# Kernel tuning notes

Hardware: AMD Instinct MI355X
Metric: run time of the kernel (lower is better)

The kernel has to match this reference:

```python
import jax, jax.numpy as jnp
import numpy as np

N, DIM, DK, DV = 8192, 1024, 128, 128


def setup_inputs() -> dict:
    key = jax.random.key(0)
    ks = jax.random.split(key, 5)
    # Match equinox Linear init scale roughly (uniform(-1/sqrt(in), 1/sqrt(in)))
    lim = 1.0 / np.sqrt(DIM)
    return {
        "x": jax.random.normal(ks[0], (N, DIM), dtype=jnp.float32),
        "Wqk": jax.random.uniform(ks[1], (DK, DIM), jnp.float32, -lim, lim),
        "bqk": jax.random.uniform(ks[2], (DK,), jnp.float32, -lim, lim),
        "Wv": jax.random.uniform(ks[3], (DV, DIM), jnp.float32, -lim, lim),
        "bv": jax.random.uniform(ks[4], (DV,), jnp.float32, -lim, lim),
    }


def reference(x, Wqk, bqk, Wv, bv):
    # shared QK projection: q == k == x @ Wqk^T + bqk  -> [n, dk]
    qk = jnp.einsum("nd,kd->nk", x, Wqk) + bqk
    v = jnp.einsum("nd,vd->nv", x, Wv) + bv  # [n, dv]
    # full n x n score matrix (no 1/sqrt(dk) scaling in the original)
    score = jnp.einsum("ik,jk->ij", qk, qk)  # [n, n]
    score = jax.nn.softmax(score, axis=-1)
    return jnp.einsum("ij,jv->iv", score, v)  # [n, dv]
```

## Files before the change

kernel.cpp:

```cpp
#include <hip/hip_runtime.h>
#include <math.h>

#define NROWS 8192
#define DIMX  1024
#define DKV   128
#define KSPLIT 4
#define KEYS_PER_SPLIT (NROWS / KSPLIT)
#define BN 64
#define QK_SCALE 1.2011224087864498f
#define M_FIX 96.0f

typedef __attribute__((ext_vector_type(8))) short bf16x8;
typedef __attribute__((ext_vector_type(4))) short s16x4;
typedef __attribute__((ext_vector_type(4))) float f32x4;

static __device__ __forceinline__ short f2bf(float f) {
    union { float f; unsigned u; } v; v.f = f;
    unsigned r = v.u + 0x7fff + ((v.u >> 16) & 1);
    return (short)(r >> 16);
}

__global__ __launch_bounds__(256) void wcvt_kernel(
    const float* __restrict__ Wqk, const float* __restrict__ bqk,
    const float* __restrict__ Wv,  const float* __restrict__ bv,
    short* __restrict__ wb, float* __restrict__ bb)
{
    const int idx = blockIdx.x * 1024 + threadIdx.x * 4;
    const bool isqk = idx < DKV * DIMX;
    const float* src = isqk ? (Wqk + idx) : (Wv + (idx - DKV * DIMX));
    const float sc = isqk ? QK_SCALE : 1.0f;
    const float4 f = *(const float4*)src;
    s16x4 o;
    o.x = f2bf(f.x * sc); o.y = f2bf(f.y * sc);
    o.z = f2bf(f.z * sc); o.w = f2bf(f.w * sc);
    *(s16x4*)&wb[idx] = o;
    if (blockIdx.x == 0) {
        const int t = threadIdx.x;
        bb[t] = (t < DKV) ? bqk[t] * QK_SCALE : bv[t - DKV];
    }
}

__global__ __launch_bounds__(256) void proj_kernel(
    const float* __restrict__ x, const short* __restrict__ wb,
    const float* __restrict__ bb, short* __restrict__ qkb, short* __restrict__ vtb)
{
    __shared__ __align__(16) short xb[32 * 1024];

    const int tid  = threadIdx.x;
    const int lane = tid & 63;
    const int wave = tid >> 6;
    const int l15  = lane & 15;
    const int quad = lane >> 4;
    const int mat  = blockIdx.y;
    const int rbase = blockIdx.x * 32;
    const int wr = wave >> 1, wc = wave & 1;
    const short* wsrc = wb + (size_t)mat * DKV * DIMX;

    #pragma unroll 8
    for (int i = 0; i < 32; ++i) {
        const float4 f = *(const float4*)(x + (size_t)(rbase + i) * DIMX + tid * 4);
        s16x4 o;
        o.x = f2bf(f.x); o.y = f2bf(f.y); o.z = f2bf(f.z); o.w = f2bf(f.w);
        *(s16x4*)&xb[i * 1024 + ((tid * 4) ^ ((i & 7) << 3))] = o;
    }
    __syncthreads();

    f32x4 acc[4];
    for (int i = 0; i < 4; ++i) acc[i] = (f32x4)0.0f;

    const int arow = wr * 16 + l15;
    const int aswz = (arow & 7) << 3;
    const short* arowp = &xb[arow * 1024];

    #pragma unroll 2
    for (int kk = 0; kk < 32; ++kk) {
        const bf16x8 a = *(const bf16x8*)&arowp[(kk * 32 + quad * 8) ^ aswz];
        for (int nt = 0; nt < 4; ++nt) {
            const int col = wc * 64 + nt * 16 + l15;
            const bf16x8 b = *(const bf16x8*)(wsrc + (size_t)col * DIMX + kk * 32 + quad * 8);
            acc[nt] = __builtin_amdgcn_mfma_f32_16x16x32_bf16(a, b, acc[nt], 0, 0, 0);
        }
    }

    const int rw = rbase + wr * 16 + quad * 4;
    for (int nt = 0; nt < 4; ++nt) {
        const int col = wc * 64 + nt * 16 + l15;
        const float bias = bb[mat * DKV + col];
        if (mat == 0) {
            for (int r = 0; r < 4; ++r)
                qkb[(size_t)(rw + r) * DKV + col] = f2bf(acc[nt][r] + bias);
        } else {
            s16x4 o;
            o.x = f2bf(acc[nt][0] + bias); o.y = f2bf(acc[nt][1] + bias);
            o.z = f2bf(acc[nt][2] + bias); o.w = f2bf(acc[nt][3] + bias);
            *(s16x4*)&vtb[(size_t)col * NROWS + rw] = o;
        }
    }
}

__global__ __launch_bounds__(256, 2) void flash_kernel(
    const short* __restrict__ qkb, const short* __restrict__ vtb,
    float* __restrict__ opart, float* __restrict__ lpart)
{
    __shared__ __align__(16) short kt[2][64 * 128];
    __shared__ __align__(16) short vt[2][128 * 64];
    __shared__ __align__(16) short pb[4][32 * 64];

    const int tid  = threadIdx.x;
    const int lane = tid & 63;
    const int wave = tid >> 6;
    const int l15  = lane & 15;
    const int quad = lane >> 4;
    const int rg   = wave >> 1;
    const int kh   = wave & 1;
    const int rbase = blockIdx.x * 64 + rg * 32;
    const int ks = blockIdx.y;
    const int swzr = (l15 & 7) << 3;

    unsigned koff[4], voff[4];
    for (int i = 0; i < 4; ++i) {
        const int krow = wave * 16 + i * 4 + quad;
        koff[i] = (unsigned)krow * 256u
                + (((unsigned)l15 * 16u) ^ (((unsigned)krow & 7u) << 4));
        const int vrow = wave * 32 + i * 8 + (lane >> 3);
        voff[i] = (unsigned)vrow * (unsigned)(NROWS * 2)
                + ((((unsigned)lane & 7u) * 16u) ^ (((unsigned)vrow & 7u) << 4));
    }

#define FL_ISSUE(buf, j0) do { \
        const char* kb_ = (const char*)qkb + (size_t)(j0) * (DKV * 2); \
        const char* vb_ = (const char*)vtb + (size_t)(j0) * 2; \
        for (int i = 0; i < 4; ++i) \
            __builtin_amdgcn_global_load_lds( \
                (const __attribute__((address_space(1))) void*)(kb_ + koff[i]), \
                (__attribute__((address_space(3))) void*)((char*)&kt[buf][0] + (wave * 4 + i) * 1024), \
                16, 0, 0); \
        for (int i = 0; i < 4; ++i) \
            __builtin_amdgcn_global_load_lds( \
                (const __attribute__((address_space(1))) void*)(vb_ + voff[i]), \
                (__attribute__((address_space(3))) void*)((char*)&vt[buf][0] + (wave * 4 + i) * 1024), \
                16, 0, 0); \
    } while (0)

    bf16x8 qf[2][4];
    #pragma unroll 2
    for (int h = 0; h < 2; ++h) {
        const short* qrow = qkb + (size_t)(rbase + h * 16 + l15) * DKV;
        for (int k = 0; k < 4; ++k)
            qf[h][k] = *(const bf16x8*)(qrow + k * 32 + quad * 8);
    }

    bf16x8 ones;
    for (int j = 0; j < 8; ++j) ones[j] = (short)0x3F80;

    f32x4 oacc[2][8];
    #pragma unroll 2
    for (int h = 0; h < 2; ++h)
        for (int i = 0; i < 8; ++i) oacc[h][i] = (f32x4)0.0f;
    f32x4 lsum[2] = {(f32x4)0.0f, (f32x4)0.0f};

    const int j_begin = ks * KEYS_PER_SPLIT;
    short* pw = &pb[wave][0];

    const int krow0 = kh * 32 + 2 * l15;
    const int swk0  = ((krow0 & 7) << 3);
    const int pxw = (quad & 1) << 6;
    const int pxr = (l15 & 4) << 4;

    FL_ISSUE(0, j_begin);
    __syncthreads();

    int cur = 0;
    for (int j0 = j_begin; j0 < j_begin + KEYS_PER_SPLIT; j0 += BN) {
        const bool more = (j0 + BN) < (j_begin + KEYS_PER_SPLIT);
        if (more) FL_ISSUE(cur ^ 1, j0 + BN);

        f32x4 s[2][2];
        __builtin_amdgcn_s_setprio(1);
        #pragma unroll 2
        for (int ntl = 0; ntl < 2; ++ntl) {
            f32x4 a0 = (f32x4)0.0f, a1 = (f32x4)0.0f;
            const int rowb = (krow0 + ntl) * 128;
            const int swk  = swk0 + ntl * 8;
            for (int k = 0; k < 4; ++k) {
                const bf16x8 b = *(const bf16x8*)
                    &kt[cur][rowb + ((k * 32 + quad * 8) ^ swk)];
                a0 = __builtin_amdgcn_mfma_f32_16x16x32_bf16(qf[0][k], b, a0, 0, 0, 0);
                a1 = __builtin_amdgcn_mfma_f32_16x16x32_bf16(qf[1][k], b, a1, 0, 0, 0);
            }
            s[0][ntl] = a0; s[1][ntl] = a1;
        }
        __builtin_amdgcn_s_setprio(0);

        #pragma unroll 2
        for (int h = 0; h < 2; ++h)
            for (int ntl = 0; ntl < 2; ++ntl)
                for (int r = 0; r < 4; ++r)
                    s[h][ntl][r] = __builtin_amdgcn_exp2f(s[h][ntl][r] - M_FIX);

        #pragma unroll 2
        for (int h = 0; h < 2; ++h)
            for (int r = 0; r < 4; ++r) {
                const int row = h * 16 + quad * 4 + r;
                unsigned pk;
                asm("v_cvt_pk_bf16_f32 %0, %1, %2" : "=v"(pk) : "v"(s[h][0][r]), "v"(s[h][1][r]));
                *(unsigned*)((char*)pw + row * 128 + ((l15 * 4) ^ pxw)) = pk;
            }

        __builtin_amdgcn_s_setprio(1);
        {
            const bf16x8 a0 = *(const bf16x8*)((char*)pw + l15 * 128 + ((quad * 16) ^ pxr));
            const bf16x8 a1 = *(const bf16x8*)((char*)pw + (16 + l15) * 128 + ((quad * 16) ^ pxr));
            lsum[0] = __builtin_amdgcn_mfma_f32_16x16x32_bf16(a0, ones, lsum[0], 0, 0, 0);
            lsum[1] = __builtin_amdgcn_mfma_f32_16x16x32_bf16(a1, ones, lsum[1], 0, 0, 0);
            for (int nt = 0; nt < 8; ++nt) {
                const bf16x8 b = *(const bf16x8*)
                    &vt[cur][(nt * 16 + l15) * 64 + ((kh * 32 + quad * 8) ^ swzr)];
                oacc[0][nt] = __builtin_amdgcn_mfma_f32_16x16x32_bf16(a0, b, oacc[0][nt], 0, 0, 0);
                oacc[1][nt] = __builtin_amdgcn_mfma_f32_16x16x32_bf16(a1, b, oacc[1][nt], 0, 0, 0);
            }
        }
        __builtin_amdgcn_s_setprio(0);

        __syncthreads();
        cur ^= 1;
    }

    float* obuf = (float*)&kt[rg][0];
    float* lbuf = (float*)&vt[0][0];
    __syncthreads();
    if (kh == 1) {
        #pragma unroll 2
        for (int h = 0; h < 2; ++h) {
            for (int nt = 0; nt < 8; ++nt)
                for (int r = 0; r < 4; ++r)
                    obuf[(h * 16 + quad * 4 + r) * 128 + nt * 16 + l15] = oacc[h][nt][r];
            if (l15 == 0)
                for (int r = 0; r < 4; ++r)
                    lbuf[rg * 32 + h * 16 + quad * 4 + r] = lsum[h][r];
        }
    }
    __syncthreads();
    if (kh == 0) {
        #pragma unroll 2
        for (int h = 0; h < 2; ++h) {
            const int rw = rbase + h * 16 + quad * 4;
            for (int nt = 0; nt < 8; ++nt) {
                const int col = nt * 16 + l15;
                for (int r = 0; r < 4; ++r)
                    opart[((size_t)ks * NROWS + rw + r) * DKV + col] =
                        oacc[h][nt][r] + obuf[(h * 16 + quad * 4 + r) * 128 + col];
            }
            if (l15 == 0)
                for (int r = 0; r < 4; ++r)
                    lpart[ks * NROWS + rw + r] =
                        lsum[h][r] + lbuf[rg * 32 + h * 16 + quad * 4 + r];
        }
    }
#undef FL_ISSUE
}

__global__ __launch_bounds__(256) void combine_kernel(
    const float* __restrict__ opart, const float* __restrict__ lpart,
    float* __restrict__ out)
{
    const int idx = blockIdx.x * 256 + threadIdx.x;
    const int row = idx >> 7;
    float L = 0.f, acc = 0.f;
    for (int s = 0; s < KSPLIT; ++s) {
        L   += lpart[s * NROWS + row];
        acc += opart[(size_t)s * NROWS * DKV + idx];
    }
    out[idx] = acc / L;
}

extern "C" void kernel_launch(void* const* d_in, const int* in_sizes, int n_in,
                              void* d_out, int out_size, void* d_ws, size_t ws_size,
                              hipStream_t stream) {
    const float* x   = (const float*)d_in[0];
    const float* Wqk = (const float*)d_in[1];
    const float* bqk = (const float*)d_in[2];
    const float* Wv  = (const float*)d_in[3];
    const float* bv  = (const float*)d_in[4];
    float* out = (float*)d_out;

    char* ws = (char*)d_ws;
    short* qkb   = (short*)ws;
    short* vtb   = (short*)(ws + (2u << 20));
    short* wb    = (short*)(ws + (4u << 20));
    float* bb    = (float*)(ws + (4u << 20) + (512u << 10));
    float* opart = (float*)(ws + (5u << 20));
    float* lpart = (float*)(ws + (21u << 20));

    wcvt_kernel<<<dim3(256), 256, 0, stream>>>(Wqk, bqk, Wv, bv, wb, bb);
    proj_kernel<<<dim3(256, 2), 256, 0, stream>>>(x, wb, bb, qkb, vtb);
    flash_kernel<<<dim3(NROWS / 64, KSPLIT), 256, 0, stream>>>(qkb, vtb, opart, lpart);
    combine_kernel<<<dim3(NROWS * DKV / 256), 256, 0, stream>>>(opart, lpart, out);
}
```

Baseline: 165.1 us.

## Load K and V fragments directly from global into registers, dropping LDS staging

The flash kernel no longer stages K and V tiles through double-buffered shared memory with global_load_lds and per-tile barriers. Each wave now loads its K fragments straight into registers, software-pipelined one tile ahead, and reads V fragments directly from global memory each tile. Shared memory is kept only for the per-wave P transpose and the final reduction. This removes the LDS traffic and block-wide syncs, but each wave now fetches data that was previously shared across the block, so global/L2 traffic rises and register pressure grows.

```diff
diff --git a/kernel.cpp b/kernel.cpp
--- a/kernel.cpp
+++ b/kernel.cpp
@@ -102,9 +102,7 @@
     const short* __restrict__ qkb, const short* __restrict__ vtb,
     float* __restrict__ opart, float* __restrict__ lpart)
 {
-    __shared__ __align__(16) short kt[2][64 * 128];
-    __shared__ __align__(16) short vt[2][128 * 64];
-    __shared__ __align__(16) short pb[4][32 * 64];
+    __shared__ __align__(16) char smem[33024];
 
     const int tid  = threadIdx.x;
     const int lane = tid & 63;
@@ -115,32 +113,8 @@
     const int kh   = wave & 1;
     const int rbase = blockIdx.x * 64 + rg * 32;
     const int ks = blockIdx.y;
-    const int swzr = (l15 & 7) << 3;
-
-    unsigned koff[4], voff[4];
-    for (int i = 0; i < 4; ++i) {
-        const int krow = wave * 16 + i * 4 + quad;
-        koff[i] = (unsigned)krow * 256u
-                + (((unsigned)l15 * 16u) ^ (((unsigned)krow & 7u) << 4));
-        const int vrow = wave * 32 + i * 8 + (lane >> 3);
-        voff[i] = (unsigned)vrow * (unsigned)(NROWS * 2)
-                + ((((unsigned)lane & 7u) * 16u) ^ (((unsigned)vrow & 7u) << 4));
-    }
-
-#define FL_ISSUE(buf, j0) do { \
-        const char* kb_ = (const char*)qkb + (size_t)(j0) * (DKV * 2); \
-        const char* vb_ = (const char*)vtb + (size_t)(j0) * 2; \
-        for (int i = 0; i < 4; ++i) \
-            __builtin_amdgcn_global_load_lds( \
-                (const __attribute__((address_space(1))) void*)(kb_ + koff[i]), \
-                (__attribute__((address_space(3))) void*)((char*)&kt[buf][0] + (wave * 4 + i) * 1024), \
-                16, 0, 0); \
-        for (int i = 0; i < 4; ++i) \
-            __builtin_amdgcn_global_load_lds( \
-                (const __attribute__((address_space(1))) void*)(vb_ + voff[i]), \
-                (__attribute__((address_space(3))) void*)((char*)&vt[buf][0] + (wave * 4 + i) * 1024), \
-                16, 0, 0); \
-    } while (0)
+
+    short* pw = (short*)(smem + wave * 4096);
 
     bf16x8 qf[2][4];
     #pragma unroll 2
@@ -159,75 +133,74 @@
         for (int i = 0; i < 8; ++i) oacc[h][i] = (f32x4)0.0f;
     f32x4 lsum[2] = {(f32x4)0.0f, (f32x4)0.0f};
 
-    const int j_begin = ks * KEYS_PER_SPLIT;
-    short* pw = &pb[wave][0];
-
-    const int krow0 = kh * 32 + 2 * l15;
-    const int swk0  = ((krow0 & 7) << 3);
+    const short* kp0 = qkb + (size_t)(kh * 32 + 2 * l15) * DKV + quad * 8;
+    const short* kp1 = kp0 + DKV;
+    const short* vp[8];
+    for (int nt = 0; nt < 8; ++nt)
+        vp[nt] = vtb + (size_t)(nt * 16 + l15) * NROWS + kh * 32 + quad * 8;
+
     const int pxw = (quad & 1) << 6;
     const int pxr = (l15 & 4) << 4;
 
-    FL_ISSUE(0, j_begin);
-    __syncthreads();
-
-    int cur = 0;
-    for (int j0 = j_begin; j0 < j_begin + KEYS_PER_SPLIT; j0 += BN) {
-        const bool more = (j0 + BN) < (j_begin + KEYS_PER_SPLIT);
-        if (more) FL_ISSUE(cur ^ 1, j0 + BN);
-
-        f32x4 s[2][2];
-        __builtin_amdgcn_s_setprio(1);
-        #pragma unroll 2
-        for (int ntl = 0; ntl < 2; ++ntl) {
-            f32x4 a0 = (f32x4)0.0f, a1 = (f32x4)0.0f;
-            const int rowb = (krow0 + ntl) * 128;
-            const int swk  = swk0 + ntl * 8;
-            for (int k = 0; k < 4; ++k) {
-                const bf16x8 b = *(const bf16x8*)
-                    &kt[cur][rowb + ((k * 32 + quad * 8) ^ swk)];
-                a0 = __builtin_amdgcn_mfma_f32_16x16x32_bf16(qf[0][k], b, a0, 0, 0, 0);
-                a1 = __builtin_amdgcn_mfma_f32_16x16x32_bf16(qf[1][k], b, a1, 0, 0, 0);
-            }
-            s[0][ntl] = a0; s[1][ntl] = a1;
-        }
-        __builtin_amdgcn_s_setprio(0);
-
-        #pragma unroll 2
-        for (int h = 0; h < 2; ++h)
-            for (int ntl = 0; ntl < 2; ++ntl)
-                for (int r = 0; r < 4; ++r)
-                    s[h][ntl][r] = __builtin_amdgcn_exp2f(s[h][ntl][r] - M_FIX);
-
-        #pragma unroll 2
-        for (int h = 0; h < 2; ++h)
-            for (int r = 0; r < 4; ++r) {
-                const int row = h * 16 + quad * 4 + r;
-                unsigned pk;
-                asm("v_cvt_pk_bf16_f32 %0, %1, %2" : "=v"(pk) : "v"(s[h][0][r]), "v"(s[h][1][r]));
-                *(unsigned*)((char*)pw + row * 128 + ((l15 * 4) ^ pxw)) = pk;
-            }
-
-        __builtin_amdgcn_s_setprio(1);
-        {
-            const bf16x8 a0 = *(const bf16x8*)((char*)pw + l15 * 128 + ((quad * 16) ^ pxr));
-            const bf16x8 a1 = *(const bf16x8*)((char*)pw + (16 + l15) * 128 + ((quad * 16) ^ pxr));
-            lsum[0] = __builtin_amdgcn_mfma_f32_16x16x32_bf16(a0, ones, lsum[0], 0, 0, 0);
-            lsum[1] = __builtin_amdgcn_mfma_f32_16x16x32_bf16(a1, ones, lsum[1], 0, 0, 0);
-            for (int nt = 0; nt < 8; ++nt) {
-                const bf16x8 b = *(const bf16x8*)
-                    &vt[cur][(nt * 16 + l15) * 64 + ((kh * 32 + quad * 8) ^ swzr)];
-                oacc[0][nt] = __builtin_amdgcn_mfma_f32_16x16x32_bf16(a0, b, oacc[0][nt], 0, 0, 0);
-                oacc[1][nt] = __builtin_amdgcn_mfma_f32_16x16x32_bf16(a1, b, oacc[1][nt], 0, 0, 0);
-            }
-        }
-        __builtin_amdgcn_s_setprio(0);
-
-        __syncthreads();
-        cur ^= 1;
-    }
-
-    float* obuf = (float*)&kt[rg][0];
-    float* lbuf = (float*)&vt[0][0];
+#define LOADK(dst, j0) do { \
+        for (int k_ = 0; k_ < 4; ++k_) { \
+            dst[0][k_] = *(const bf16x8*)(kp0 + (size_t)(j0) * DKV + k_ * 32); \
+            dst[1][k_] = *(const bf16x8*)(kp1 + (size_t)(j0) * DKV + k_ * 32); \
+        } } while (0)
+
+#define TILE(KC, KN, j0, more) do { \
+        bf16x8 vf[8]; \
+        for (int nt = 0; nt < 8; ++nt) \
+            vf[nt] = *(const bf16x8*)(vp[nt] + (j0)); \
+        f32x4 s[2][2]; \
+        __builtin_amdgcn_s_setprio(1); \
+        for (int ntl = 0; ntl < 2; ++ntl) { \
+            f32x4 a0 = (f32x4)0.0f, a1 = (f32x4)0.0f; \
+            for (int k_ = 0; k_ < 4; ++k_) { \
+                a0 = __builtin_amdgcn_mfma_f32_16x16x32_bf16(qf[0][k_], KC[ntl][k_], a0, 0, 0, 0); \
+                a1 = __builtin_amdgcn_mfma_f32_16x16x32_bf16(qf[1][k_], KC[ntl][k_], a1, 0, 0, 0); \
+            } \
+            s[0][ntl] = a0; s[1][ntl] = a1; \
+        } \
+        __builtin_amdgcn_s_setprio(0); \
+        for (int h = 0; h < 2; ++h) \
+            for (int ntl = 0; ntl < 2; ++ntl) \
+                for (int r = 0; r < 4; ++r) \
+                    s[h][ntl][r] = __builtin_amdgcn_exp2f(s[h][ntl][r] - M_FIX); \
+        for (int h = 0; h < 2; ++h) \
+            for (int r = 0; r < 4; ++r) { \
+                const int row = h * 16 + quad * 4 + r; \
+                unsigned pk; \
+                asm("v_cvt_pk_bf16_f32 %0, %1, %2" : "=v"(pk) : "v"(s[h][0][r]), "v"(s[h][1][r])); \
+                *(unsigned*)(pw ? (char*)pw + row * 128 + ((l15 * 4) ^ pxw) : 0) = pk; \
+            } \
+        if (more) LOADK(KN, (j0) + BN); \
+        __builtin_amdgcn_s_setprio(1); \
+        { \
+            const bf16x8 a0 = *(const bf16x8*)((char*)pw + l15 * 128 + ((quad * 16) ^ pxr)); \
+            const bf16x8 a1 = *(const bf16x8*)((char*)pw + (16 + l15) * 128 + ((quad * 16) ^ pxr)); \
+            lsum[0] = __builtin_amdgcn_mfma_f32_16x16x32_bf16(a0, ones, lsum[0], 0, 0, 0); \
+            lsum[1] = __builtin_amdgcn_mfma_f32_16x16x32_bf16(a1, ones, lsum[1], 0, 0, 0); \
+            for (int nt = 0; nt < 8; ++nt) { \
+                oacc[0][nt] = __builtin_amdgcn_mfma_f32_16x16x32_bf16(a0, vf[nt], oacc[0][nt], 0, 0, 0); \
+                oacc[1][nt] = __builtin_amdgcn_mfma_f32_16x16x32_bf16(a1, vf[nt], oacc[1][nt], 0, 0, 0); \
+            } \
+        } \
+        __builtin_amdgcn_s_setprio(0); \
+    } while (0)
+
+    const int j_begin = ks * KEYS_PER_SPLIT;
+    const int j_end   = j_begin + KEYS_PER_SPLIT;
+
+    bf16x8 kfA[2][4], kfB[2][4];
+    LOADK(kfA, j_begin);
+    for (int j0 = j_begin; j0 < j_end; j0 += 2 * BN) {
+        TILE(kfA, kfB, j0, true);
+        TILE(kfB, kfA, j0 + BN, (j0 + 2 * BN) < j_end);
+    }
+
+    float* obuf = (float*)smem + rg * 32 * 128;
+    float* lbuf = (float*)(smem + 32768);
     __syncthreads();
     if (kh == 1) {
         #pragma unroll 2
@@ -257,7 +230,8 @@
                         lsum[h][r] + lbuf[rg * 32 + h * 16 + quad * 4 + r];
         }
     }
-#undef FL_ISSUE
+#undef LOADK
+#undef TILE
 }
 
 __global__ __launch_bounds__(256) void combine_kernel(
```

New measurement: 234.5 us. 1.42x slower.
